# Optimization experiments

Hardware: AMD Instinct MI355X
Metric: run time of the kernel (lower is better)

Reference implementation:

```python
import jax, jax.numpy as jnp
import numpy as np

B, T, D = 8, 4096, 1024

def setup_inputs() -> dict:
    key = jax.random.key(0)
    k1, k2, k3, k4, k5 = jax.random.split(key, 5)
    s = 1.0 / np.sqrt(D)
    return {
        "seq": jax.random.normal(k1, (B, T, D), dtype=jnp.float32),
        "W_delta": jax.random.uniform(k2, (D, D), jnp.float32, -s, s),
        "b_delta": jax.random.uniform(k3, (D,), jnp.float32, -s, s),
        "W_value": jax.random.uniform(k4, (D, D), jnp.float32, -s, s),
        "b_value": jax.random.uniform(k5, (D,), jnp.float32, -s, s),
    }

def reference(seq, W_delta, b_delta, W_value, b_value):
    # delta = sigmoid(seq @ W_delta^T + b_delta); value = seq @ W_value^T + b_value
    delta = jax.nn.sigmoid(jnp.einsum("btd,ed->bte", seq, W_delta) + b_delta)
    value = jnp.einsum("btd,ed->bte", seq, W_value) + b_value
    # gated linear recurrence: state_t = (1-delta_t)*state_{t-1} + delta_t*value_t
    def step(state, dv):
        d, v = dv  # each [B, D]
        state = (1.0 - d) * state + d * v
        return state, state
    init = jnp.zeros((seq.shape[0], seq.shape[-1]), dtype=seq.dtype)
    # time-major for scan
    _, out = jax.lax.scan(step, init, (delta.transpose(1, 0, 2), value.transpose(1, 0, 2)))
    return out.transpose(1, 0, 2)  # [B, T, D]
```

## Files before the change

kernel.cpp:

```cpp
#include <hip/hip_runtime.h>
#include <hip/hip_bf16.h>


typedef _Float16 f16;
typedef _Float16 f16x8 __attribute__((ext_vector_type(8)));
typedef float    f32x4 __attribute__((ext_vector_type(4)));

#define NB  8
#define NT  4096
#define ND  1024
#define NM  (NB*NT)
#define KK  2048
#define NKT 32

#define CT  128
#define NCH (NT/CT)

#define OFF_AP     0UL
#define OFF_BP     134217728UL
#define OFF_VALUE  142606336UL
#define OFF_AARR   276824064UL
#define OFF_SARR   277872640UL
#define OFF_SIN    278921216UL

#define GLOAD_LDS16(gp, lp)                                                          \
  __builtin_amdgcn_global_load_lds(                                                  \
      (const __attribute__((address_space(1))) void*)(gp),                           \
      (__attribute__((address_space(3))) void*)(lp), 16, 0, 0)

#define MEMFENCE asm volatile("" ::: "memory")
#define BARRIER() do { MEMFENCE; __builtin_amdgcn_s_barrier(); MEMFENCE; } while (0)
#define WAITV2() asm volatile("s_waitcnt vmcnt(2)" ::: "memory")
#define WAITV0() asm volatile("s_waitcnt vmcnt(0)" ::: "memory")

__global__ void k_convert_seq(const float* __restrict__ src, f16* __restrict__ Ap) {
  const long n8 = (long)NM * ND / 8;
  long i = (long)blockIdx.x * blockDim.x + threadIdx.x;
  const long stride = (long)gridDim.x * blockDim.x;
  for (; i < n8; i += stride) {
    const long m = i >> 7;
    const int k8 = ((int)i & 127) * 8;
    const float4 v0 = *(const float4*)(src + m * ND + k8);
    const float4 v1 = *(const float4*)(src + m * ND + k8 + 4);
    const float a[8] = {v0.x, v0.y, v0.z, v0.w, v1.x, v1.y, v1.z, v1.w};
    f16x8 hi, lo;
#pragma unroll
    for (int j = 0; j < 8; ++j) {
      const f16 h = (f16)a[j];
      hi[j] = h;
      lo[j] = (f16)(a[j] - (float)h);
    }
    *(f16x8*)(Ap + m * KK + k8) = hi;
    *(f16x8*)(Ap + m * KK + ND + k8) = lo;
  }
}

__global__ void k_convert_w(const float* __restrict__ Wd, const float* __restrict__ Wv,
                            f16* __restrict__ Bp) {
  const long i = (long)blockIdx.x * blockDim.x + threadIdx.x;
  const int n = (int)(i >> 7);
  const int k8 = ((int)i & 127) * 8;
  const float* row = (n < ND) ? (Wd + (long)n * ND) : (Wv + (long)(n - ND) * ND);
  const float4 v0 = *(const float4*)(row + k8);
  const float4 v1 = *(const float4*)(row + k8 + 4);
  const float a[8] = {v0.x, v0.y, v0.z, v0.w, v1.x, v1.y, v1.z, v1.w};
  f16x8 h;
#pragma unroll
  for (int j = 0; j < 8; ++j) h[j] = (f16)a[j];
  *(f16x8*)(Bp + (long)n * ND + k8) = h;
}

#define LDS_A(c) ((c) * 65536)
#define LDS_B(c) ((c) * 65536 + 32768)

__global__ __launch_bounds__(512, 2) void k_gemm(
    const f16* __restrict__ Ap, const f16* __restrict__ Bp,
    const float* __restrict__ bd, const float* __restrict__ bv,
    float* __restrict__ dOut, float* __restrict__ vOut) {
  __shared__ char smem[131072];

  const int t = threadIdx.x;
  const int w = t >> 6, lane = t & 63;
  const int wr = w >> 2, wc = w & 3;
  const int l15 = lane & 15, l4 = lane >> 4;

  const int bid = blockIdx.x;
  const int sw = (bid & 7) * 128 + (bid >> 3);
  const int bm = sw >> 3, bn = sw & 7;
  const long m0 = (long)bm * 256;
  const int n0 = bn * 256;

  f32x4 acc[8][4] = {};

  const int rl0 = t >> 3;
  const int rl1 = 64 + (t >> 3);
  const int c16_0 = (t & 7) ^ (rl0 & 7);
  const int c16_1 = (t & 7) ^ (rl1 & 7);

  auto stageA = [&](int kt, int h, int c) {
    const f16* s0 = Ap + (m0 + h * 128 + rl0) * (long)KK + kt * 64 + c16_0 * 8;
    const f16* s1 = Ap + (m0 + h * 128 + rl1) * (long)KK + kt * 64 + c16_1 * 8;
    char* base = smem + LDS_A(c) + h * 16384 + w * 1024;
    GLOAD_LDS16(s0, base);
    GLOAD_LDS16(s1, base + 8192);
  };
  auto stageB = [&](int kt, int h, int c) {
    const int kb = (kt & 15) * 64;
    const f16* s0 = Bp + (long)(n0 + h * 128 + rl0) * ND + kb + c16_0 * 8;
    const f16* s1 = Bp + (long)(n0 + h * 128 + rl1) * ND + kb + c16_1 * 8;
    char* base = smem + LDS_B(c) + h * 16384 + w * 1024;
    GLOAD_LDS16(s0, base);
    GLOAD_LDS16(s1, base + 8192);
  };

  f16x8 aF[8], bF[2];
  auto readA = [&](int c, int k) {
#pragma unroll
    for (int mf = 0; mf < 8; ++mf) {
      const int row = wr * 128 + mf * 16 + l15;
      const int c16 = (k * 4 + l4) ^ (row & 7);
      aF[mf] = *(const f16x8*)(smem + LDS_A(c) + row * 128 + c16 * 16);
    }
  };
  auto readB = [&](int c, int k, int nh) {
#pragma unroll
    for (int nfl = 0; nfl < 2; ++nfl) {
      const int row = nh * 128 + wc * 32 + nfl * 16 + l15;
      const int c16 = (k * 4 + l4) ^ (row & 7);
      bF[nfl] = *(const f16x8*)(smem + LDS_B(c) + row * 128 + c16 * 16);
    }
  };
  auto mfmaQ = [&](int nh) {
    __builtin_amdgcn_s_setprio(1);
#pragma unroll
    for (int mf = 0; mf < 8; ++mf)
#pragma unroll
      for (int nfl = 0; nfl < 2; ++nfl)
        acc[mf][nh * 2 + nfl] = __builtin_amdgcn_mfma_f32_16x16x32_f16(
            aF[mf], bF[nfl], acc[mf][nh * 2 + nfl], 0, 0, 0);
    __builtin_amdgcn_s_setprio(0);
  };

  auto tile = [&](int c, int ktNext, bool pf) {
    if (pf) stageA(ktNext, 0, c ^ 1);
    readA(c, 0); readB(c, 0, 0);
    BARRIER();
    mfmaQ(0);
    if (pf) { WAITV2(); } else { WAITV0(); }
    BARRIER();
    if (pf) stageA(ktNext, 1, c ^ 1);
    readB(c, 0, 1);
    BARRIER();
    mfmaQ(1);
    BARRIER();
    if (pf) stageB(ktNext, 0, c ^ 1);
    readA(c, 1); readB(c, 1, 0);
    BARRIER();
    mfmaQ(0);
    BARRIER();
    if (pf) stageB(ktNext, 1, c ^ 1);
    readB(c, 1, 1);
    BARRIER();
    mfmaQ(1);
    if (pf) { WAITV2(); } else { WAITV0(); }
    BARRIER();
  };

  stageA(0, 0, 0); stageA(0, 1, 0); stageB(0, 0, 0); stageB(0, 1, 0);
  WAITV2();
  BARRIER();

  for (int i = 0; i < 16; ++i) {
    tile(0, 2 * i + 1, true);
    tile(1, 2 * i + 2, i < 15);
  }

  const bool isDelta = (n0 < ND);
#pragma unroll
  for (int nf = 0; nf < 4; ++nf) {
    const int sr = (nf >> 1) * 128 + wc * 32 + (nf & 1) * 16 + l15;
    const int n = n0 + sr;
    const float bias = isDelta ? bd[n] : bv[n - ND];
#pragma unroll
    for (int mf = 0; mf < 8; ++mf) {
#pragma unroll
      for (int r = 0; r < 4; ++r) {
        const long m = m0 + wr * 128 + mf * 16 + l4 * 4 + r;
        const float x = acc[mf][nf][r] + bias;
        if (isDelta)
          dOut[m * ND + n] = 1.0f / (1.0f + __expf(-x));
        else
          vOut[m * ND + (n - ND)] = x;
      }
    }
  }
}

__global__ void k_scan_local(const float* __restrict__ delta, const float* __restrict__ value,
                             float* __restrict__ Aarr, float* __restrict__ Sarr) {
  const int bid = blockIdx.x;
  const int dg = bid & 3, c = (bid >> 2) & 31, b = bid >> 7;
  const int d = dg * 256 + threadIdx.x;
  const long base = ((long)b * NT + (long)c * CT) * ND + d;
  float a = 1.0f, s = 0.0f;
#pragma unroll 4
  for (int tt = 0; tt < CT; ++tt) {
    const float dl = delta[base + (long)tt * ND];
    const float v  = value[base + (long)tt * ND];
    const float om = 1.0f - dl;
    a *= om;
    s = om * s + dl * v;
  }
  const int idx = (b * NCH + c) * ND + d;
  Aarr[idx] = a;
  Sarr[idx] = s;
}

__global__ void k_scan_prefix(const float* __restrict__ Aarr, const float* __restrict__ Sarr,
                              float* __restrict__ Sin) {
  const int tid = blockIdx.x * blockDim.x + threadIdx.x;
  const int b = tid >> 10, d = tid & 1023;
  float st = 0.0f;
  for (int c = 0; c < NCH; ++c) {
    const int idx = (b * NCH + c) * ND + d;
    Sin[idx] = st;
    st = Aarr[idx] * st + Sarr[idx];
  }
}

__global__ void k_scan_apply(const float* __restrict__ value, const float* __restrict__ Sin,
                             float* __restrict__ out) {
  const int bid = blockIdx.x;
  const int dg = bid & 3, c = (bid >> 2) & 31, b = bid >> 7;
  const int d = dg * 256 + threadIdx.x;
  const long base = ((long)b * NT + (long)c * CT) * ND + d;
  float st = Sin[(b * NCH + c) * ND + d];
#pragma unroll 4
  for (int tt = 0; tt < CT; ++tt) {
    const long idx = base + (long)tt * ND;
    const float dl = out[idx];
    const float v  = value[idx];
    st = (1.0f - dl) * st + dl * v;
    out[idx] = st;
  }
}

extern "C" void kernel_launch(void* const* d_in, const int* in_sizes, int n_in,
                              void* d_out, int out_size, void* d_ws, size_t ws_size,
                              hipStream_t stream) {
  const float* seq = (const float*)d_in[0];
  const float* Wd  = (const float*)d_in[1];
  const float* bd  = (const float*)d_in[2];
  const float* Wv  = (const float*)d_in[3];
  const float* bv  = (const float*)d_in[4];
  float* out = (float*)d_out;

  char* ws = (char*)d_ws;
  f16*   Ap    = (f16*)(ws + OFF_AP);
  f16*   Bp    = (f16*)(ws + OFF_BP);
  float* value = (float*)(ws + OFF_VALUE);
  float* Aarr  = (float*)(ws + OFF_AARR);
  float* Sarr  = (float*)(ws + OFF_SARR);
  float* Sin   = (float*)(ws + OFF_SIN);

  hipLaunchKernelGGL(k_convert_seq, dim3(2048), dim3(256), 0, stream, seq, Ap);
  hipLaunchKernelGGL(k_convert_w,   dim3(1024), dim3(256), 0, stream, Wd, Wv, Bp);
  hipLaunchKernelGGL(k_gemm, dim3(1024), dim3(512), 0, stream, Ap, Bp, bd, bv, out, value);
  hipLaunchKernelGGL(k_scan_local,  dim3(1024), dim3(256), 0, stream, out, value, Aarr, Sarr);
  hipLaunchKernelGGL(k_scan_prefix, dim3(32),   dim3(256), 0, stream, Aarr, Sarr, Sin);
  hipLaunchKernelGGL(k_scan_apply,  dim3(1024), dim3(256), 0, stream, value, Sin, out);
}
```

Before: 627.3 us.

## Transpose MFMA operands for vectorized GEMM epilogue and vectorize scan kernels with float4

Swaps the A/B operands of the MFMA so each lane holds four consecutive output columns, which lets the GEMM epilogue load bias as a float4 and store delta/value as 16-byte vectors instead of scattered scalar stores. The three scan kernels now process four channels per thread with float4 loads and stores, and the grid is cut by four. The aim is fewer, wider memory transactions. The tradeoff is lower parallelism in the memory-bound scan kernels: 256 blocks instead of 1024, and 8 prefix blocks instead of 32.

```diff
diff --git a/kernel.cpp b/kernel.cpp
--- a/kernel.cpp
+++ b/kernel.cpp
@@ -11,7 +11,6 @@
 #define ND  1024
 #define NM  (NB*NT)
 #define KK  2048
-#define NKT 32
 
 #define CT  128
 #define NCH (NT/CT)
@@ -137,7 +136,7 @@
 #pragma unroll
       for (int nfl = 0; nfl < 2; ++nfl)
         acc[mf][nh * 2 + nfl] = __builtin_amdgcn_mfma_f32_16x16x32_f16(
-            aF[mf], bF[nfl], acc[mf][nh * 2 + nfl], 0, 0, 0);
+            bF[nfl], aF[mf], acc[mf][nh * 2 + nfl], 0, 0, 0);
     __builtin_amdgcn_s_setprio(0);
   };
 
@@ -178,19 +177,19 @@
   const bool isDelta = (n0 < ND);
 #pragma unroll
   for (int nf = 0; nf < 4; ++nf) {
-    const int sr = (nf >> 1) * 128 + wc * 32 + (nf & 1) * 16 + l15;
-    const int n = n0 + sr;
-    const float bias = isDelta ? bd[n] : bv[n - ND];
+    const int nb = n0 + (nf >> 1) * 128 + wc * 32 + (nf & 1) * 16 + l4 * 4;
+    const float4 bias = *(const float4*)(isDelta ? (bd + nb) : (bv + (nb - ND)));
 #pragma unroll
     for (int mf = 0; mf < 8; ++mf) {
-#pragma unroll
-      for (int r = 0; r < 4; ++r) {
-        const long m = m0 + wr * 128 + mf * 16 + l4 * 4 + r;
-        const float x = acc[mf][nf][r] + bias;
-        if (isDelta)
-          dOut[m * ND + n] = 1.0f / (1.0f + __expf(-x));
-        else
-          vOut[m * ND + (n - ND)] = x;
+      const long m = m0 + wr * 128 + mf * 16 + l15;
+      f32x4 x = acc[mf][nf];
+      x[0] += bias.x; x[1] += bias.y; x[2] += bias.z; x[3] += bias.w;
+      if (isDelta) {
+#pragma unroll
+        for (int r = 0; r < 4; ++r) x[r] = 1.0f / (1.0f + __expf(-x[r]));
+        *(f32x4*)(dOut + m * ND + nb) = x;
+      } else {
+        *(f32x4*)(vOut + m * ND + (nb - ND)) = x;
       }
     }
   }
@@ -199,49 +198,61 @@
 __global__ void k_scan_local(const float* __restrict__ delta, const float* __restrict__ value,
                              float* __restrict__ Aarr, float* __restrict__ Sarr) {
   const int bid = blockIdx.x;
-  const int dg = bid & 3, c = (bid >> 2) & 31, b = bid >> 7;
-  const int d = dg * 256 + threadIdx.x;
+  const int c = bid & 31, b = bid >> 5;
+  const int d = threadIdx.x * 4;
   const long base = ((long)b * NT + (long)c * CT) * ND + d;
-  float a = 1.0f, s = 0.0f;
+  float4 a = make_float4(1.f, 1.f, 1.f, 1.f);
+  float4 s = make_float4(0.f, 0.f, 0.f, 0.f);
 #pragma unroll 4
   for (int tt = 0; tt < CT; ++tt) {
-    const float dl = delta[base + (long)tt * ND];
-    const float v  = value[base + (long)tt * ND];
-    const float om = 1.0f - dl;
-    a *= om;
-    s = om * s + dl * v;
-  }
-  const int idx = (b * NCH + c) * ND + d;
-  Aarr[idx] = a;
-  Sarr[idx] = s;
+    const float4 dl = *(const float4*)(delta + base + (long)tt * ND);
+    const float4 v  = *(const float4*)(value + base + (long)tt * ND);
+    const float o0 = 1.0f - dl.x, o1 = 1.0f - dl.y, o2 = 1.0f - dl.z, o3 = 1.0f - dl.w;
+    a.x *= o0; a.y *= o1; a.z *= o2; a.w *= o3;
+    s.x = o0 * s.x + dl.x * v.x;
+    s.y = o1 * s.y + dl.y * v.y;
+    s.z = o2 * s.z + dl.z * v.z;
+    s.w = o3 * s.w + dl.w * v.w;
+  }
+  const long o = (long)(b * NCH + c) * ND + d;
+  *(float4*)(Aarr + o) = a;
+  *(float4*)(Sarr + o) = s;
 }
 
 __global__ void k_scan_prefix(const float* __restrict__ Aarr, const float* __restrict__ Sarr,
                               float* __restrict__ Sin) {
   const int tid = blockIdx.x * blockDim.x + threadIdx.x;
-  const int b = tid >> 10, d = tid & 1023;
-  float st = 0.0f;
+  const int b = tid >> 8, d = (tid & 255) * 4;
+  float4 st = make_float4(0.f, 0.f, 0.f, 0.f);
   for (int c = 0; c < NCH; ++c) {
-    const int idx = (b * NCH + c) * ND + d;
-    Sin[idx] = st;
-    st = Aarr[idx] * st + Sarr[idx];
+    const long idx = (long)(b * NCH + c) * ND + d;
+    *(float4*)(Sin + idx) = st;
+    const float4 a = *(const float4*)(Aarr + idx);
+    const float4 s = *(const float4*)(Sarr + idx);
+    st.x = a.x * st.x + s.x;
+    st.y = a.y * st.y + s.y;
+    st.z = a.z * st.z + s.z;
+    st.w = a.w * st.w + s.w;
   }
 }
 
 __global__ void k_scan_apply(const float* __restrict__ value, const float* __restrict__ Sin,
                              float* __restrict__ out) {
   const int bid = blockIdx.x;
-  const int dg = bid & 3, c = (bid >> 2) & 31, b = bid >> 7;
-  const int d = dg * 256 + threadIdx.x;
+  const int c = bid & 31, b = bid >> 5;
+  const int d = threadIdx.x * 4;
   const long base = ((long)b * NT + (long)c * CT) * ND + d;
-  float st = Sin[(b * NCH + c) * ND + d];
+  float4 st = *(const float4*)(Sin + (long)(b * NCH + c) * ND + d);
 #pragma unroll 4
   for (int tt = 0; tt < CT; ++tt) {
     const long idx = base + (long)tt * ND;
-    const float dl = out[idx];
-    const float v  = value[idx];
-    st = (1.0f - dl) * st + dl * v;
-    out[idx] = st;
+    const float4 dl = *(const float4*)(out + idx);
+    const float4 v  = *(const float4*)(value + idx);
+    st.x = (1.0f - dl.x) * st.x + dl.x * v.x;
+    st.y = (1.0f - dl.y) * st.y + dl.y * v.y;
+    st.z = (1.0f - dl.z) * st.z + dl.z * v.z;
+    st.w = (1.0f - dl.w) * st.w + dl.w * v.w;
+    *(float4*)(out + idx) = st;
   }
 }
 
@@ -266,7 +277,7 @@
   hipLaunchKernelGGL(k_convert_seq, dim3(2048), dim3(256), 0, stream, seq, Ap);
   hipLaunchKernelGGL(k_convert_w,   dim3(1024), dim3(256), 0, stream, Wd, Wv, Bp);
   hipLaunchKernelGGL(k_gemm, dim3(1024), dim3(512), 0, stream, Ap, Bp, bd, bv, out, value);
-  hipLaunchKernelGGL(k_scan_local,  dim3(1024), dim3(256), 0, stream, out, value, Aarr, Sarr);
-  hipLaunchKernelGGL(k_scan_prefix, dim3(32),   dim3(256), 0, stream, Aarr, Sarr, Sin);
-  hipLaunchKernelGGL(k_scan_apply,  dim3(1024), dim3(256), 0, stream, value, Sin, out);
-}
+  hipLaunchKernelGGL(k_scan_local,  dim3(256), dim3(256), 0, stream, out, value, Aarr, Sarr);
+  hipLaunchKernelGGL(k_scan_prefix, dim3(8),   dim3(256), 0, stream, Aarr, Sarr, Sin);
+  hipLaunchKernelGGL(k_scan_apply,  dim3(256), dim3(256), 0, stream, value, Sin, out);
+}
```

Result: no change. 624.4 us (-0.5%).
